# Kernel tuning notes

Measured on AMD Instinct MI355X. Metric: run time of the kernel, lower is better.

## Reference

```python
import jax, jax.numpy as jnp
import numpy as np

D_MODEL = 768
STATE_N = 16
BATCH = 8
SEQ = 2048


def setup_inputs() -> dict:
    key = jax.random.key(0)
    ks = jax.random.split(key, 12)
    d, n = D_MODEL, STATE_N
    s = 0.02
    inp = {
        "x": jax.random.normal(ks[0], (BATCH, SEQ, d), dtype=jnp.float32),
        # A_log init as in module: log(arange(1..N)) repeated over d_model
        "A_log": jnp.log(jnp.tile(jnp.arange(1, n + 1, dtype=jnp.float32)[None, :], (d, 1))),
        "D_param": jnp.ones((d,), dtype=jnp.float32),
        "B_proj_w": jax.random.normal(ks[1], (n, d), dtype=jnp.float32) * s,
        "C_proj_w": jax.random.normal(ks[2], (n, d), dtype=jnp.float32) * s,
        "delta_w": jax.random.normal(ks[3], (d, d), dtype=jnp.float32) * s,
        "delta_b": jax.random.normal(ks[4], (d,), dtype=jnp.float32) * s,
        "in_w": jax.random.normal(ks[5], (2 * d, d), dtype=jnp.float32) * s,
        "in_b": jax.random.normal(ks[6], (2 * d,), dtype=jnp.float32) * s,
        "out_w": jax.random.normal(ks[7], (d, d), dtype=jnp.float32) * s,
        "out_b": jax.random.normal(ks[8], (d,), dtype=jnp.float32) * s,
        "conv_w": jax.random.normal(ks[9], (d, 1, 3), dtype=jnp.float32) * s,  # depthwise [D,1,K]
        "conv_b": jax.random.normal(ks[10], (d,), dtype=jnp.float32) * s,
    }
    return inp


def _forward(x, A_log, D_param, B_proj_w, C_proj_w, delta_w, delta_b,
             in_w, in_b, out_w, out_b, conv_w, conv_b):
    A = -jnp.exp(A_log)  # [D, N]
    xz = jnp.einsum("bld,ed->ble", x, in_w) + in_b  # [B, L, 2D]
    x_in, z = jnp.split(xz, 2, axis=-1)
    # depthwise conv1d, padding=1, groups=D (cross-correlation, same as torch)
    x_c = jax.lax.conv_general_dilated(
        jnp.transpose(x_in, (0, 2, 1)), conv_w,
        window_strides=(1,), padding=((1, 1),),
        feature_group_count=x.shape[-1],
        dimension_numbers=("NCH", "OIH", "NCH"))
    x_conv = jnp.transpose(x_c, (0, 2, 1)) + conv_b  # [B, L, D]
    x_conv = jax.nn.silu(x_conv)
    delta = jax.nn.softplus(jnp.einsum("bld,ed->ble", x_conv, delta_w) + delta_b)  # [B,L,D]
    B_sel = jnp.einsum("bld,nd->bln", x_conv, B_proj_w)  # [B, L, N]
    C_sel = jnp.einsum("bld,nd->bln", x_conv, C_proj_w)  # [B, L, N]

    Bsz, L, D = x.shape
    N = A.shape[1]

    def step(h, t_in):
        dt, b_t, c_t, x_t = t_in  # [B,D], [B,N], [B,N], [B,D]
        A_bar = jnp.exp(dt[:, :, None] * A[None, :, :])           # [B,D,N]
        h = A_bar * h + (dt[:, :, None] * b_t[:, None, :]) * x_t[:, :, None]
        y_t = jnp.sum(h * c_t[:, None, :], axis=-1)               # [B,D]
        return h, y_t

    xs = (jnp.transpose(delta, (1, 0, 2)), jnp.transpose(B_sel, (1, 0, 2)),
          jnp.transpose(C_sel, (1, 0, 2)), jnp.transpose(x_conv, (1, 0, 2)))
    h0 = jnp.zeros((Bsz, D, N), dtype=x.dtype)
    _, ys = jax.lax.scan(step, h0, xs)
    y = jnp.transpose(ys, (1, 0, 2))  # [B, L, D]

    y = y + x_conv * D_param[None, None, :]
    y = y * jax.nn.silu(z)
    return jnp.einsum("bld,ed->ble", y, out_w) + out_b


def reference(x, A_log, D_param, B_proj_w, C_proj_w, delta_w, delta_b,
              in_w, in_b, out_w, out_b, conv_w, conv_b):
    return _forward(x, A_log, D_param, B_proj_w, C_proj_w, delta_w, delta_b,
                    in_w, in_b, out_w, out_b, conv_w, conv_b)
```

## Files before the change

### kernel.cpp

```cpp
#include <hip/hip_runtime.h>
#include <hip/hip_bf16.h>

#define D_MODEL 768
#define SEQL    2048
#define BATCH   8
#define NSTATE  16
#define NCHUNK  32
#define TCHUNK  64

typedef __attribute__((ext_vector_type(8))) short short8;
typedef __attribute__((ext_vector_type(4))) float f32x4;

typedef const __attribute__((address_space(1))) unsigned int gas1_t;
typedef __attribute__((address_space(3))) unsigned int las3_t;

__device__ __forceinline__ void gload_lds16(const void* g, void* l) {
  __builtin_amdgcn_global_load_lds((gas1_t*)g, (las3_t*)l, 16, 0, 0);
}

__global__ __launch_bounds__(256) void f32_to_bf16_x4(const float* __restrict__ in,
                                                      __hip_bfloat16* __restrict__ out) {
  int i = (blockIdx.x * 256 + threadIdx.x) * 4;
  float4 v = *(const float4*)(in + i);
  out[i + 0] = __float2bfloat16(v.x);
  out[i + 1] = __float2bfloat16(v.y);
  out[i + 2] = __float2bfloat16(v.z);
  out[i + 3] = __float2bfloat16(v.w);
}

__global__ __launch_bounds__(256) void prep_weights(
    const float* __restrict__ in_w, const float* __restrict__ delta_w,
    const float* __restrict__ Bp, const float* __restrict__ Cp,
    const float* __restrict__ out_w, const float* __restrict__ A_log,
    __hip_bfloat16* __restrict__ w_in, __hip_bfloat16* __restrict__ w_dbc,
    __hip_bfloat16* __restrict__ w_out, float* __restrict__ A2) {
  int i = blockIdx.x * 256 + threadIdx.x;
  if (i < 1536 * 768) { w_in[i] = __float2bfloat16(in_w[i]); return; }
  i -= 1536 * 768;
  if (i < 896 * 768) {
    int row = i / 768, col = i - row * 768;
    float v;
    if (row < 768)      v = delta_w[row * 768 + col];
    else if (row < 784) v = Bp[(row - 768) * 768 + col];
    else if (row < 800) v = Cp[(row - 784) * 768 + col];
    else                v = 0.f;
    w_dbc[i] = __float2bfloat16(v);
    return;
  }
  i -= 896 * 768;
  if (i < 768 * 768) { w_out[i] = __float2bfloat16(out_w[i]); return; }
  i -= 768 * 768;
  if (i < 768 * 16) A2[i] = -expf(A_log[i]) * 1.44269504088896f;
}

template <int MODE>
__global__ __launch_bounds__(256) void gemm_bt(
    const __hip_bfloat16* __restrict__ A, const __hip_bfloat16* __restrict__ Bw,
    const float* __restrict__ bias, void* __restrict__ out0,
    void* __restrict__ out1, void* __restrict__ out2, int K) {
  __shared__ __hip_bfloat16 sA[128 * 32];
  __shared__ __hip_bfloat16 sB[128 * 32];
  const int tid  = threadIdx.x;
  const int lane = tid & 63, wave = tid >> 6;
  const int wr = wave >> 1, wc = wave & 1;
  const int rowA0 = blockIdx.y * 128;
  const int rowB0 = blockIdx.x * 128;

  f32x4 acc[4][4] = {};

  for (int kt = 0; kt < K; kt += 32) {
    __syncthreads();
#pragma unroll
    for (int s = 0; s < 2; ++s) {
      const unsigned off = s * 4096 + tid * 16;
      const unsigned r = off >> 6, cb = off & 63;
      gload_lds16((const char*)(A + (size_t)(rowA0 + r) * K + kt) + cb,
                  (char*)sA + off);
      gload_lds16((const char*)(Bw + (size_t)(rowB0 + r) * K + kt) + cb,
                  (char*)sB + off);
    }
    __syncthreads();

    short8 a[4], b[4];
#pragma unroll
    for (int m = 0; m < 4; ++m)
      a[m] = *(const short8*)((const char*)sA + (wr * 64 + m * 16 + (lane & 15)) * 64 +
                              ((lane >> 4) << 4));
#pragma unroll
    for (int n = 0; n < 4; ++n)
      b[n] = *(const short8*)((const char*)sB + (wc * 64 + n * 16 + (lane & 15)) * 64 +
                              ((lane >> 4) << 4));
#pragma unroll
    for (int m = 0; m < 4; ++m)
#pragma unroll
      for (int n = 0; n < 4; ++n)
        acc[m][n] = __builtin_amdgcn_mfma_f32_16x16x32_bf16(a[m], b[n], acc[m][n], 0, 0, 0);
  }

#pragma unroll
  for (int m = 0; m < 4; ++m) {
    const int grow_base = rowA0 + wr * 64 + m * 16 + ((lane >> 4) << 2);
#pragma unroll
    for (int n = 0; n < 4; ++n) {
      const int gcol = rowB0 + wc * 64 + n * 16 + (lane & 15);
#pragma unroll
      for (int i = 0; i < 4; ++i) {
        const size_t grow = grow_base + i;
        float v = acc[m][n][i];
        if (MODE == 0) {
          v += bias[gcol];
          if (gcol < 768)
            ((__hip_bfloat16*)out0)[grow * 768 + gcol] = __float2bfloat16(v);
          else
            ((__hip_bfloat16*)out1)[grow * 768 + gcol - 768] = __float2bfloat16(v);
        } else if (MODE == 1) {
          if (gcol < 768) {
            v += bias[gcol];
            float sp = (v > 20.f) ? v : log1pf(expf(v));
            ((float*)out0)[grow * 768 + gcol] = sp;
          } else if (gcol < 784) {
            ((float*)out1)[grow * 16 + (gcol - 768)] = v;
          } else if (gcol < 800) {
            ((float*)out2)[grow * 16 + (gcol - 784)] = v;
          }
        } else {
          ((float*)out0)[grow * 768 + gcol] = v + bias[gcol];
        }
      }
    }
  }
}

__global__ __launch_bounds__(256) void conv_silu(
    const __hip_bfloat16* __restrict__ xin, const float* __restrict__ conv_w,
    const float* __restrict__ conv_b, __hip_bfloat16* __restrict__ xc) {
  const int idx = blockIdx.x * 256 + threadIdx.x;
  const int d = idx % 768;
  const int t = (idx / 768) % SEQL;
  const float w0 = conv_w[d * 3], w1 = conv_w[d * 3 + 1], w2 = conv_w[d * 3 + 2];
  float acc = conv_b[d];
  float xm = (t > 0)        ? __bfloat162float(xin[idx - 768]) : 0.f;
  float x0 = __bfloat162float(xin[idx]);
  float xp = (t < SEQL - 1) ? __bfloat162float(xin[idx + 768]) : 0.f;
  acc += w0 * xm + w1 * x0 + w2 * xp;
  const float sig = 1.f / (1.f + __expf(-acc));
  xc[idx] = __float2bfloat16(acc * sig);
}

__global__ __launch_bounds__(256) void scan_pass1(
    const float* __restrict__ delta, const __hip_bfloat16* __restrict__ xconv,
    const float* __restrict__ Bsel, const float* __restrict__ A2,
    float* __restrict__ sumdt, float* __restrict__ Sbuf) {
  const int d = blockIdx.x * 256 + threadIdx.x;
  const int b = blockIdx.y, c = blockIdx.z;
  __shared__ float sB[TCHUNK * 16];
  ((float4*)sB)[threadIdx.x] =
      ((const float4*)(Bsel + ((size_t)b * SEQL + c * TCHUNK) * 16))[threadIdx.x];
  __syncthreads();

  float a2[16];
#pragma unroll
  for (int n = 0; n < 16; ++n) a2[n] = A2[d * 16 + n];
  float h[16] = {};
  float sdt = 0.f;
  const size_t base = ((size_t)b * SEQL + c * TCHUNK) * 768 + d;
  for (int t = 0; t < TCHUNK; ++t) {
    const float dt = delta[base + (size_t)t * 768];
    const float x = __bfloat162float(xconv[base + (size_t)t * 768]);
    sdt += dt;
    const float dtx = dt * x;
    const float* Br = &sB[t * 16];
#pragma unroll
    for (int n = 0; n < 16; ++n) {
      const float a = exp2f(dt * a2[n]);
      h[n] = fmaf(a, h[n], dtx * Br[n]);
    }
  }
  sumdt[((size_t)b * NCHUNK + c) * 768 + d] = sdt;
#pragma unroll
  for (int n = 0; n < 16; ++n)
    Sbuf[(((size_t)b * NCHUNK + c) * 16 + n) * 768 + d] = h[n];
}

__global__ __launch_bounds__(256) void scan_carry(
    const float* __restrict__ sumdt, const float* __restrict__ Sbuf,
    const float* __restrict__ A2, float* __restrict__ Hin) {
  const int idx = blockIdx.x * 256 + threadIdx.x;
  const int b = idx / 768, d = idx - b * 768;
  float a2[16];
#pragma unroll
  for (int n = 0; n < 16; ++n) a2[n] = A2[d * 16 + n];
  float h[16] = {};
  for (int c = 0; c < NCHUNK; ++c) {
    const size_t hb = ((size_t)b * NCHUNK + c) * 16 * 768 + d;
#pragma unroll
    for (int n = 0; n < 16; ++n) Hin[hb + (size_t)n * 768] = h[n];
    const float sd = sumdt[((size_t)b * NCHUNK + c) * 768 + d];
#pragma unroll
    for (int n = 0; n < 16; ++n) {
      const float P = exp2f(sd * a2[n]);
      h[n] = fmaf(P, h[n], Sbuf[hb + (size_t)n * 768]);
    }
  }
}

__global__ __launch_bounds__(256) void scan_pass3(
    const float* __restrict__ delta, const __hip_bfloat16* __restrict__ xconv,
    const __hip_bfloat16* __restrict__ zb, const float* __restrict__ Bsel,
    const float* __restrict__ Csel, const float* __restrict__ A2,
    const float* __restrict__ Hin, const float* __restrict__ Dp,
    __hip_bfloat16* __restrict__ yg) {
  const int d = blockIdx.x * 256 + threadIdx.x;
  const int b = blockIdx.y, c = blockIdx.z;
  __shared__ float sB[TCHUNK * 16], sC[TCHUNK * 16];
  {
    const size_t off = ((size_t)b * SEQL + c * TCHUNK) * 16;
    ((float4*)sB)[threadIdx.x] = ((const float4*)(Bsel + off))[threadIdx.x];
    ((float4*)sC)[threadIdx.x] = ((const float4*)(Csel + off))[threadIdx.x];
  }
  __syncthreads();

  float a2[16];
#pragma unroll
  for (int n = 0; n < 16; ++n) a2[n] = A2[d * 16 + n];
  float h[16];
  {
    const size_t hb = ((size_t)b * NCHUNK + c) * 16 * 768 + d;
#pragma unroll
    for (int n = 0; n < 16; ++n) h[n] = Hin[hb + (size_t)n * 768];
  }
  const float Dpd = Dp[d];
  const size_t base = ((size_t)b * SEQL + c * TCHUNK) * 768 + d;
  for (int t = 0; t < TCHUNK; ++t) {
    const float dt = delta[base + (size_t)t * 768];
    const float x = __bfloat162float(xconv[base + (size_t)t * 768]);
    const float dtx = dt * x;
    const float* Br = &sB[t * 16];
    const float* Cr = &sC[t * 16];
    float y = 0.f;
#pragma unroll
    for (int n = 0; n < 16; ++n) {
      const float a = exp2f(dt * a2[n]);
      h[n] = fmaf(a, h[n], dtx * Br[n]);
      y = fmaf(h[n], Cr[n], y);
    }
    const float z = __bfloat162float(zb[base + (size_t)t * 768]);
    const float sig = 1.f / (1.f + __expf(-z));
    const float out = (y + x * Dpd) * (z * sig);
    yg[base + (size_t)t * 768] = __float2bfloat16(out);
  }
}

extern "C" void kernel_launch(void* const* d_in, const int* in_sizes, int n_in,
                              void* d_out, int out_size, void* d_ws, size_t ws_size,
                              hipStream_t stream) {
  const float* x       = (const float*)d_in[0];
  const float* A_log   = (const float*)d_in[1];
  const float* D_param = (const float*)d_in[2];
  const float* B_proj  = (const float*)d_in[3];
  const float* C_proj  = (const float*)d_in[4];
  const float* delta_w = (const float*)d_in[5];
  const float* delta_b = (const float*)d_in[6];
  const float* in_w    = (const float*)d_in[7];
  const float* in_b    = (const float*)d_in[8];
  const float* out_w   = (const float*)d_in[9];
  const float* out_b   = (const float*)d_in[10];
  const float* conv_w  = (const float*)d_in[11];
  const float* conv_b  = (const float*)d_in[12];

  char* ws = (char*)d_ws;
  __hip_bfloat16* xb      = (__hip_bfloat16*)(ws + 0);
  __hip_bfloat16* w_in_b  = (__hip_bfloat16*)(ws + 25165824);
  __hip_bfloat16* w_dbc_b = (__hip_bfloat16*)(ws + 27525120);
  __hip_bfloat16* w_out_b = (__hip_bfloat16*)(ws + 28901376);
  float*          A2      = (float*)(ws + 30081024);
  __hip_bfloat16* xin_b   = (__hip_bfloat16*)(ws + 30130176);
  __hip_bfloat16* z_b     = (__hip_bfloat16*)(ws + 55296000);
  __hip_bfloat16* xconv_b = (__hip_bfloat16*)(ws + 80461824);
  float*          delta_f = (float*)(ws + 105627648);
  float*          Bsel    = (float*)(ws + 155959296);
  float*          Csel    = (float*)(ws + 157007872);
  float*          sumdt   = (float*)(ws + 158056448);
  float*          Sbuf    = (float*)(ws + 158842880);
  float*          Hin     = (float*)(ws + 171425792);
  __hip_bfloat16* yg      = (__hip_bfloat16*)(ws + 184008704);

  const int BLD = BATCH * SEQL * D_MODEL;

  f32_to_bf16_x4<<<BLD / 4 / 256, 256, 0, stream>>>(x, xb);
  prep_weights<<<(1536 * 768 + 896 * 768 + 768 * 768 + 768 * 16) / 256, 256, 0, stream>>>(
      in_w, delta_w, B_proj, C_proj, out_w, A_log, w_in_b, w_dbc_b, w_out_b, A2);
  gemm_bt<0><<<dim3(12, 128), 256, 0, stream>>>(xb, w_in_b, in_b, xin_b, z_b, nullptr, 768);
  conv_silu<<<BLD / 256, 256, 0, stream>>>(xin_b, conv_w, conv_b, xconv_b);
  gemm_bt<1><<<dim3(7, 128), 256, 0, stream>>>(xconv_b, w_dbc_b, delta_b, delta_f, Bsel, Csel, 768);
  scan_pass1<<<dim3(3, BATCH, NCHUNK), 256, 0, stream>>>(delta_f, xconv_b, Bsel, A2, sumdt, Sbuf);
  scan_carry<<<24, 256, 0, stream>>>(sumdt, Sbuf, A2, Hin);
  scan_pass3<<<dim3(3, BATCH, NCHUNK), 256, 0, stream>>>(delta_f, xconv_b, z_b, Bsel, Csel, A2,
                                                         Hin, D_param, yg);
  gemm_bt<2><<<dim3(6, 128), 256, 0, stream>>>(yg, w_out_b, out_b, (float*)d_out, nullptr,
                                               nullptr, 768);
}
```

Measured before the change: 426.0 us.

## Replace GEMM with 256x256-tile double-buffered swizzled-LDS MFMA kernel

The three linear-projection GEMMs now use a new 512-thread kernel with 256x256 output tiles, K-step 64, double-buffered LDS staging through global_load_lds, XOR-swizzled LDS layout, workgroup index swizzling and s_setprio around the MFMA bursts. The delta/B/C weight matrix is padded to 1024 rows so it fits the larger tile, and the yg buffer now reuses the xb workspace. The goal is more data reuse per tile and overlap of global loads with MFMA work. In exchange the grids are much smaller (192-384 blocks), each block uses 128KB of LDS so occupancy drops, and the padded rows add wasted MFMA work in the delta GEMM.

```diff
diff --git a/kernel.cpp b/kernel.cpp
--- a/kernel.cpp
+++ b/kernel.cpp
@@ -37,7 +37,7 @@
   int i = blockIdx.x * 256 + threadIdx.x;
   if (i < 1536 * 768) { w_in[i] = __float2bfloat16(in_w[i]); return; }
   i -= 1536 * 768;
-  if (i < 896 * 768) {
+  if (i < 1024 * 768) {
     int row = i / 768, col = i - row * 768;
     float v;
     if (row < 768)      v = delta_w[row * 768 + col];
@@ -47,88 +47,169 @@
     w_dbc[i] = __float2bfloat16(v);
     return;
   }
-  i -= 896 * 768;
+  i -= 1024 * 768;
   if (i < 768 * 768) { w_out[i] = __float2bfloat16(out_w[i]); return; }
   i -= 768 * 768;
   if (i < 768 * 16) A2[i] = -expf(A_log[i]) * 1.44269504088896f;
 }
 
 template <int MODE>
-__global__ __launch_bounds__(256) void gemm_bt(
-    const __hip_bfloat16* __restrict__ A, const __hip_bfloat16* __restrict__ Bw,
+__global__ __launch_bounds__(512) void gemm256(
+    const __hip_bfloat16* __restrict__ Amat, const __hip_bfloat16* __restrict__ Bw,
     const float* __restrict__ bias, void* __restrict__ out0,
-    void* __restrict__ out1, void* __restrict__ out2, int K) {
-  __shared__ __hip_bfloat16 sA[128 * 32];
-  __shared__ __hip_bfloat16 sB[128 * 32];
+    void* __restrict__ out1, void* __restrict__ out2,
+    const int K, const int gxn) {
+  __shared__ char lds[131072];
   const int tid  = threadIdx.x;
   const int lane = tid & 63, wave = tid >> 6;
-  const int wr = wave >> 1, wc = wave & 1;
-  const int rowA0 = blockIdx.y * 128;
-  const int rowB0 = blockIdx.x * 128;
-
-  f32x4 acc[4][4] = {};
-
-  for (int kt = 0; kt < K; kt += 32) {
-    __syncthreads();
-#pragma unroll
-    for (int s = 0; s < 2; ++s) {
-      const unsigned off = s * 4096 + tid * 16;
-      const unsigned r = off >> 6, cb = off & 63;
-      gload_lds16((const char*)(A + (size_t)(rowA0 + r) * K + kt) + cb,
-                  (char*)sA + off);
-      gload_lds16((const char*)(Bw + (size_t)(rowB0 + r) * K + kt) + cb,
-                  (char*)sB + off);
-    }
-    __syncthreads();
-
-    short8 a[4], b[4];
-#pragma unroll
-    for (int m = 0; m < 4; ++m)
-      a[m] = *(const short8*)((const char*)sA + (wr * 64 + m * 16 + (lane & 15)) * 64 +
-                              ((lane >> 4) << 4));
-#pragma unroll
-    for (int n = 0; n < 4; ++n)
-      b[n] = *(const short8*)((const char*)sB + (wc * 64 + n * 16 + (lane & 15)) * 64 +
-                              ((lane >> 4) << 4));
-#pragma unroll
-    for (int m = 0; m < 4; ++m)
-#pragma unroll
-      for (int n = 0; n < 4; ++n)
-        acc[m][n] = __builtin_amdgcn_mfma_f32_16x16x32_bf16(a[m], b[n], acc[m][n], 0, 0, 0);
-  }
-
-#pragma unroll
-  for (int m = 0; m < 4; ++m) {
-    const int grow_base = rowA0 + wr * 64 + m * 16 + ((lane >> 4) << 2);
-#pragma unroll
-    for (int n = 0; n < 4; ++n) {
-      const int gcol = rowB0 + wc * 64 + n * 16 + (lane & 15);
-#pragma unroll
-      for (int i = 0; i < 4; ++i) {
-        const size_t grow = grow_base + i;
-        float v = acc[m][n][i];
-        if (MODE == 0) {
-          v += bias[gcol];
-          if (gcol < 768)
-            ((__hip_bfloat16*)out0)[grow * 768 + gcol] = __float2bfloat16(v);
-          else
-            ((__hip_bfloat16*)out1)[grow * 768 + gcol - 768] = __float2bfloat16(v);
-        } else if (MODE == 1) {
-          if (gcol < 768) {
-            v += bias[gcol];
-            float sp = (v > 20.f) ? v : log1pf(expf(v));
-            ((float*)out0)[grow * 768 + gcol] = sp;
-          } else if (gcol < 784) {
-            ((float*)out1)[grow * 16 + (gcol - 768)] = v;
-          } else if (gcol < 800) {
-            ((float*)out2)[grow * 16 + (gcol - 784)] = v;
+  const int wr = wave >> 2, wc = wave & 3;
+
+  const int nwg = gridDim.x;
+  const int id  = blockIdx.x;
+  const int swz = (id & 7) * (nwg >> 3) + (id >> 3);
+  const int tm = swz / gxn, tn = swz % gxn;
+  const int rowA0 = tm * 256, rowB0 = tn * 256;
+
+  const int srow = tid >> 3;
+  const int scol = ((((tid & 7) << 4) ^ ((srow & 7) << 4)) >> 1);
+  const __hip_bfloat16* gA = Amat + (size_t)(rowA0 + srow) * K + scol;
+  const __hip_bfloat16* gB = Bw   + (size_t)(rowB0 + srow) * K + scol;
+  const int ldst = tid << 4;
+
+  const int frow = lane & 15;
+  const int fq   = lane >> 4;
+  const int fswz = (lane & 7) << 4;
+  const int pc0 = ((fq << 4)) ^ fswz;
+  const int pc1 = (64 | (fq << 4)) ^ fswz;
+  const int aro = (wr * 128 + frow) * 128;
+  const int bro = (wc * 64 + frow) * 128;
+
+  f32x4 acc[2][2][4][2];
+#pragma unroll
+  for (int mh = 0; mh < 2; ++mh)
+#pragma unroll
+    for (int nh = 0; nh < 2; ++nh)
+#pragma unroll
+      for (int m = 0; m < 4; ++m)
+#pragma unroll
+        for (int n = 0; n < 2; ++n) acc[mh][nh][m][n] = (f32x4){0.f, 0.f, 0.f, 0.f};
+
+#define STAGE_A(buf, kt)                                                        \
+  {                                                                             \
+    const __hip_bfloat16* sp = gA + (size_t)(kt) * 64;                          \
+    char* dp = lds + ((buf) << 15) + ldst;                                      \
+    _Pragma("unroll") for (int ss = 0; ss < 4; ++ss)                            \
+        gload_lds16(sp + (size_t)(ss * 64) * K, dp + ss * 8192);                \
+  }
+#define STAGE_B(buf, kt)                                                        \
+  {                                                                             \
+    const __hip_bfloat16* sp = gB + (size_t)(kt) * 64;                          \
+    char* dp = lds + 65536 + ((buf) << 15) + ldst;                              \
+    _Pragma("unroll") for (int ss = 0; ss < 4; ++ss)                            \
+        gload_lds16(sp + (size_t)(ss * 64) * K, dp + ss * 8192);                \
+  }
+
+  short8 a[4][2], b[2][2];
+#define LOADA(sAp, mh)                                                          \
+  {                                                                             \
+    _Pragma("unroll") for (int m = 0; m < 4; ++m) {                             \
+      const char* p = (sAp) + aro + ((mh)*64 + m * 16) * 128;                   \
+      a[m][0] = *(const short8*)(p + pc0);                                      \
+      a[m][1] = *(const short8*)(p + pc1);                                      \
+    }                                                                           \
+  }
+#define LOADB(sBp, nh)                                                          \
+  {                                                                             \
+    _Pragma("unroll") for (int n = 0; n < 2; ++n) {                             \
+      const char* p = (sBp) + bro + ((nh)*32 + n * 16) * 128;                   \
+      b[n][0] = *(const short8*)(p + pc0);                                      \
+      b[n][1] = *(const short8*)(p + pc1);                                      \
+    }                                                                           \
+  }
+#define MMA(mh, nh)                                                             \
+  {                                                                             \
+    __builtin_amdgcn_s_setprio(1);                                              \
+    _Pragma("unroll") for (int m = 0; m < 4; ++m)                               \
+    _Pragma("unroll") for (int n = 0; n < 2; ++n)                               \
+    _Pragma("unroll") for (int ks = 0; ks < 2; ++ks)                            \
+        acc[mh][nh][m][n] = __builtin_amdgcn_mfma_f32_16x16x32_bf16(            \
+            a[m][ks], b[n][ks], acc[mh][nh][m][n], 0, 0, 0);                    \
+    __builtin_amdgcn_s_setprio(0);                                              \
+  }
+
+  STAGE_A(0, 0);
+  STAGE_B(0, 0);
+  asm volatile("s_waitcnt vmcnt(0)" ::: "memory");
+  __builtin_amdgcn_s_barrier();
+
+  const int NT = K >> 6;
+  for (int kt = 0; kt < NT; ++kt) {
+    const int cur = kt & 1, nxt = cur ^ 1;
+    char* sA = lds + (cur << 15);
+    char* sB = lds + 65536 + (cur << 15);
+    const bool st = (kt + 1 < NT);
+    LOADA(sA, 0);
+    LOADB(sB, 0);
+    if (st) STAGE_A(nxt, kt + 1);
+    __builtin_amdgcn_s_barrier();
+    MMA(0, 0);
+    __builtin_amdgcn_s_barrier();
+    LOADB(sB, 1);
+    if (st) STAGE_B(nxt, kt + 1);
+    __builtin_amdgcn_s_barrier();
+    MMA(0, 1);
+    __builtin_amdgcn_s_barrier();
+    LOADA(sA, 1);
+    __builtin_amdgcn_s_barrier();
+    MMA(1, 1);
+    __builtin_amdgcn_s_barrier();
+    LOADB(sB, 0);
+    __builtin_amdgcn_s_barrier();
+    MMA(1, 0);
+    asm volatile("s_waitcnt vmcnt(0)" ::: "memory");
+    __builtin_amdgcn_s_barrier();
+  }
+
+#pragma unroll
+  for (int mh = 0; mh < 2; ++mh)
+#pragma unroll
+    for (int nh = 0; nh < 2; ++nh)
+#pragma unroll
+      for (int m = 0; m < 4; ++m)
+#pragma unroll
+        for (int n = 0; n < 2; ++n) {
+          const int grow0 = rowA0 + wr * 128 + mh * 64 + m * 16 + fq * 4;
+          const int gcol  = rowB0 + wc * 64 + nh * 32 + n * 16 + frow;
+#pragma unroll
+          for (int i = 0; i < 4; ++i) {
+            const size_t grow = grow0 + i;
+            float v = acc[mh][nh][m][n][i];
+            if (MODE == 0) {
+              v += bias[gcol];
+              if (gcol < 768)
+                ((__hip_bfloat16*)out0)[grow * 768 + gcol] = __float2bfloat16(v);
+              else
+                ((__hip_bfloat16*)out1)[grow * 768 + gcol - 768] = __float2bfloat16(v);
+            } else if (MODE == 1) {
+              if (gcol < 768) {
+                v += bias[gcol];
+                float sp = (v > 20.f) ? v : log1pf(expf(v));
+                ((float*)out0)[grow * 768 + gcol] = sp;
+              } else if (gcol < 784) {
+                ((float*)out1)[grow * 16 + (gcol - 768)] = v;
+              } else if (gcol < 800) {
+                ((float*)out2)[grow * 16 + (gcol - 784)] = v;
+              }
+            } else {
+              ((float*)out0)[grow * 768 + gcol] = v + bias[gcol];
+            }
           }
-        } else {
-          ((float*)out0)[grow * 768 + gcol] = v + bias[gcol];
         }
-      }
-    }
-  }
+#undef STAGE_A
+#undef STAGE_B
+#undef LOADA
+#undef LOADB
+#undef MMA
 }
 
 __global__ __launch_bounds__(256) void conv_silu(
@@ -272,31 +353,30 @@
   __hip_bfloat16* xb      = (__hip_bfloat16*)(ws + 0);
   __hip_bfloat16* w_in_b  = (__hip_bfloat16*)(ws + 25165824);
   __hip_bfloat16* w_dbc_b = (__hip_bfloat16*)(ws + 27525120);
-  __hip_bfloat16* w_out_b = (__hip_bfloat16*)(ws + 28901376);
-  float*          A2      = (float*)(ws + 30081024);
-  __hip_bfloat16* xin_b   = (__hip_bfloat16*)(ws + 30130176);
-  __hip_bfloat16* z_b     = (__hip_bfloat16*)(ws + 55296000);
-  __hip_bfloat16* xconv_b = (__hip_bfloat16*)(ws + 80461824);
-  float*          delta_f = (float*)(ws + 105627648);
-  float*          Bsel    = (float*)(ws + 155959296);
-  float*          Csel    = (float*)(ws + 157007872);
-  float*          sumdt   = (float*)(ws + 158056448);
-  float*          Sbuf    = (float*)(ws + 158842880);
-  float*          Hin     = (float*)(ws + 171425792);
-  __hip_bfloat16* yg      = (__hip_bfloat16*)(ws + 184008704);
+  __hip_bfloat16* w_out_b = (__hip_bfloat16*)(ws + 29097984);
+  float*          A2      = (float*)(ws + 30277632);
+  __hip_bfloat16* xin_b   = (__hip_bfloat16*)(ws + 30326784);
+  __hip_bfloat16* z_b     = (__hip_bfloat16*)(ws + 55492608);
+  __hip_bfloat16* xconv_b = (__hip_bfloat16*)(ws + 80658432);
+  float*          delta_f = (float*)(ws + 105824256);
+  float*          Bsel    = (float*)(ws + 156155904);
+  float*          Csel    = (float*)(ws + 157204480);
+  float*          sumdt   = (float*)(ws + 158253056);
+  float*          Sbuf    = (float*)(ws + 159039488);
+  float*          Hin     = (float*)(ws + 171622400);
+  __hip_bfloat16* yg      = xb;
 
   const int BLD = BATCH * SEQL * D_MODEL;
 
   f32_to_bf16_x4<<<BLD / 4 / 256, 256, 0, stream>>>(x, xb);
-  prep_weights<<<(1536 * 768 + 896 * 768 + 768 * 768 + 768 * 16) / 256, 256, 0, stream>>>(
+  prep_weights<<<(1536 * 768 + 1024 * 768 + 768 * 768 + 768 * 16) / 256, 256, 0, stream>>>(
       in_w, delta_w, B_proj, C_proj, out_w, A_log, w_in_b, w_dbc_b, w_out_b, A2);
-  gemm_bt<0><<<dim3(12, 128), 256, 0, stream>>>(xb, w_in_b, in_b, xin_b, z_b, nullptr, 768);
+  gemm256<0><<<384, 512, 0, stream>>>(xb, w_in_b, in_b, xin_b, z_b, nullptr, 768, 6);
   conv_silu<<<BLD / 256, 256, 0, stream>>>(xin_b, conv_w, conv_b, xconv_b);
-  gemm_bt<1><<<dim3(7, 128), 256, 0, stream>>>(xconv_b, w_dbc_b, delta_b, delta_f, Bsel, Csel, 768);
+  gemm256<1><<<256, 512, 0, stream>>>(xconv_b, w_dbc_b, delta_b, delta_f, Bsel, Csel, 768, 4);
   scan_pass1<<<dim3(3, BATCH, NCHUNK), 256, 0, stream>>>(delta_f, xconv_b, Bsel, A2, sumdt, Sbuf);
   scan_carry<<<24, 256, 0, stream>>>(sumdt, Sbuf, A2, Hin);
   scan_pass3<<<dim3(3, BATCH, NCHUNK), 256, 0, stream>>>(delta_f, xconv_b, z_b, Bsel, Csel, A2,
                                                          Hin, D_param, yg);
-  gemm_bt<2><<<dim3(6, 128), 256, 0, stream>>>(yg, w_out_b, out_b, (float*)d_out, nullptr,
-                                               nullptr, 768);
-}
+  gemm256<2><<<192, 512, 0, stream>>>(yg, w_out_b, out_b, (float*)d_out, nullptr, nullptr, 768, 3);
+}
```

New measurement: 399.0 us. 1.07x faster.
